# Performance work log

Measured on AMD Instinct MI355X. Metric: run time of the kernel, lower is better.

Reference implementation:

```python
import jax, jax.numpy as jnp
import numpy as np

H, W = 64, 64
C = 256
NH = 8
WS = 8
SS = 4
N = WS * WS
HD = C // NH
HIDDEN = 4 * C
CPB_HIDDEN = 512
EPS = 1e-6


def _window_partition(x, ws):
    B, H_, W_, C_ = x.shape
    x = x.reshape(B, H_ // ws, ws, W_ // ws, ws, C_).transpose(0, 1, 3, 2, 4, 5)
    return x.reshape(-1, ws, ws, C_)


def _window_reverse(win, ws, H_, W_):
    B = win.shape[0] // ((H_ // ws) * (W_ // ws))
    x = win.reshape(B, H_ // ws, W_ // ws, ws, ws, -1).transpose(0, 1, 3, 2, 4, 5)
    return x.reshape(B, H_, W_, -1)


def _coords_table():
    # (1, 2*WS-1, 2*WS-1, 2) log-spaced continuous relative coords (SwinV2 CPB)
    ch = np.arange(-(WS - 1), WS)
    cw = np.arange(-(WS - 1), WS)
    t = np.stack(np.meshgrid(ch, cw, indexing='ij'), axis=-1)[None].astype(np.float32)
    t = t / (WS - 1) * 8.0
    t = np.sign(t) * np.log2(np.abs(t) + 1.0) / np.log2(8.0)
    return t.astype(np.float32)


def _rpe_index():
    coords = np.stack(np.meshgrid(np.arange(WS), np.arange(WS), indexing='ij'))
    cf = coords.reshape(2, -1)
    rel = (cf[:, :, None] - cf[:, None, :]).transpose(1, 2, 0)
    rel[:, :, 0] += WS - 1
    rel[:, :, 1] += WS - 1
    rel[:, :, 0] *= 2 * WS - 1
    return rel.sum(-1)  # (N, N) int


def _attn_mask():
    img = np.zeros((1, H, W, 1), np.float32)
    cnt = 0
    for hs in (slice(0, -WS), slice(-WS, -SS), slice(-SS, None)):
        for ws_ in (slice(0, -WS), slice(-WS, -SS), slice(-SS, None)):
            img[:, hs, ws_, :] = cnt
            cnt += 1
    mw = img.reshape(1, H // WS, WS, W // WS, WS, 1).transpose(0, 1, 3, 2, 4, 5).reshape(-1, N)
    am = mw[:, None, :] - mw[:, :, None]
    return np.where(am != 0, -100.0, 0.0).astype(np.float32)  # (nW, N, N)


_TABLE = jnp.asarray(_coords_table())
_RPE = jnp.asarray(_rpe_index().reshape(-1))
_AMASK = jnp.asarray(_attn_mask())


def setup_inputs() -> dict:
    key = jax.random.key(0)
    ks = jax.random.split(key, 12)
    s = 0.02
    return {
        'x': jax.random.normal(ks[0], (32, H * W, C), jnp.float32),
        'qkv_w': jax.random.normal(ks[1], (C, 3 * C), jnp.float32) * s,
        'q_bias': jnp.zeros((C,), jnp.float32),
        'v_bias': jnp.zeros((C,), jnp.float32),
        'logit_scale': jnp.log(10.0 * jnp.ones((NH, 1, 1), jnp.float32)),
        'cpb_w1': jax.random.normal(ks[2], (2, CPB_HIDDEN), jnp.float32) * s,
        'cpb_b1': jnp.zeros((CPB_HIDDEN,), jnp.float32),
        'cpb_w2': jax.random.normal(ks[3], (CPB_HIDDEN, NH), jnp.float32) * s,
        'proj_w': jax.random.normal(ks[4], (C, C), jnp.float32) * s,
        'proj_b': jnp.zeros((C,), jnp.float32),
        'norm1_scale': jnp.ones((C,), jnp.float32),
        'norm1_bias': jnp.zeros((C,), jnp.float32),
        'norm2_scale': jnp.ones((C,), jnp.float32),
        'norm2_bias': jnp.zeros((C,), jnp.float32),
        'fc1_w': jax.random.normal(ks[5], (C, HIDDEN), jnp.float32) * s,
        'fc1_b': jnp.zeros((HIDDEN,), jnp.float32),
        'fc2_w': jax.random.normal(ks[6], (HIDDEN, C), jnp.float32) * s,
        'fc2_b': jnp.zeros((C,), jnp.float32),
    }


def _layernorm(y, scale, bias):
    mu = jnp.mean(y, axis=-1, keepdims=True)
    var = jnp.mean(jnp.square(y - mu), axis=-1, keepdims=True)
    return (y - mu) * jax.lax.rsqrt(var + EPS) * scale + bias


def _l2n(t):
    return t * jax.lax.rsqrt(jnp.maximum(jnp.sum(t * t, axis=-1, keepdims=True), 1e-12))


def reference(x, qkv_w, q_bias, v_bias, logit_scale, cpb_w1, cpb_b1, cpb_w2,
              proj_w, proj_b, norm1_scale, norm1_bias, norm2_scale, norm2_bias,
              fc1_w, fc1_b, fc2_w, fc2_b):
    B, L, C_ = x.shape
    nW = _AMASK.shape[0]
    shortcut = x

    # cyclic shift + window partition
    xi = x.reshape(B, H, W, C_)
    xi = jnp.roll(xi, (-SS, -SS), axis=(1, 2))
    xw = _window_partition(xi, WS).reshape(-1, N, C_)  # (B_, N, C)
    B_ = xw.shape[0]

    # qkv with q/v bias only (k bias is zero)
    qkv_bias = jnp.concatenate([q_bias, jnp.zeros_like(v_bias), v_bias])
    qkv = xw @ qkv_w + qkv_bias
    qkv = qkv.reshape(B_, N, 3, NH, HD).transpose(2, 0, 3, 1, 4)
    q, k, v = qkv[0], qkv[1], qkv[2]  # (B_, NH, N, HD)

    # cosine attention with learned clamped logit scale
    attn = jnp.einsum('bhnd,bhmd->bhnm', _l2n(q), _l2n(k))
    scale = jnp.exp(jnp.minimum(logit_scale, np.log(100.0)))  # (NH,1,1)
    attn = attn * scale

    # continuous-position-bias MLP -> relative position bias, 16*sigmoid
    bias_table = jax.nn.relu(_TABLE @ cpb_w1 + cpb_b1) @ cpb_w2  # (1,2WS-1,2WS-1,NH)
    bias_table = bias_table.reshape(-1, NH)
    rpb = bias_table[_RPE].reshape(N, N, NH).transpose(2, 0, 1)  # (NH,N,N)
    attn = attn + (16.0 * jax.nn.sigmoid(rpb))[None]

    # shifted-window mask
    attn = attn.reshape(B_ // nW, nW, NH, N, N) + _AMASK[None, :, None]
    attn = jax.nn.softmax(attn.reshape(B_, NH, N, N), axis=-1)

    out = jnp.einsum('bhnm,bhmd->bnhd', attn, v).reshape(B_, N, C_)
    out = out @ proj_w + proj_b

    # window reverse + reverse cyclic shift
    out = _window_reverse(out.reshape(-1, WS, WS, C_), WS, H, W)
    out = jnp.roll(out, (SS, SS), axis=(1, 2)).reshape(B, L, C_)

    # SwinV2 post-norm residuals
    x1 = shortcut + _layernorm(out, norm1_scale, norm1_bias)
    h = jax.nn.gelu(x1 @ fc1_w + fc1_b) @ fc2_w + fc2_b
    return x1 + _layernorm(h, norm2_scale, norm2_bias)
```

## Files before the change

kernel.cpp:

```cpp
#include <hip/hip_runtime.h>

typedef __bf16 bf16;
typedef __bf16 bf16x8 __attribute__((ext_vector_type(8)));
typedef __bf16 bf16x4 __attribute__((ext_vector_type(4)));
typedef float  f32x4  __attribute__((ext_vector_type(4)));

#define MFMA16(a, b, c) __builtin_amdgcn_mfma_f32_16x16x32_bf16(a, b, c, 0, 0, 0)

__device__ __forceinline__ void gload_lds16(const void* g, void* l) {
    __builtin_amdgcn_global_load_lds((const __attribute__((address_space(1))) void*)g,
                                     (__attribute__((address_space(3))) void*)l, 16, 0, 0);
}

__device__ __forceinline__ long win2orig(long r) {
    long b = r >> 12; int rem = (int)(r & 4095);
    int widx = rem >> 6, t = rem & 63;
    int rp = ((widx >> 3) << 3) + (t >> 3), cp = ((widx & 7) << 3) + (t & 7);
    int rr = (rp + 4) & 63, cc = (cp + 4) & 63;
    return (b << 12) + rr * 64 + cc;
}

template <int GELU>
__global__ __launch_bounds__(256) void gemm_bt(const bf16* __restrict__ A,
                                               const bf16* __restrict__ Bt,
                                               const float* __restrict__ bias,
                                               bf16* __restrict__ C,
                                               int M, int N, int K) {
    __shared__ bf16 As[4096];
    __shared__ bf16 Bs[4096];
    const int t = threadIdx.x;
    const int w = t >> 6, l = t & 63;
    const int l15 = l & 15, q4 = l >> 4;
    const int wm = w >> 1, wn = w & 1;
    const long row0 = (long)blockIdx.y * 128;
    const int col0 = blockIdx.x * 128;

    const bf16* aP = A + (row0 + w * 16 + l15) * (long)K + q4 * 8;
    const bf16* bP = Bt + (long)(col0 + w * 16 + l15) * K + q4 * 8;
    const long step64 = 64L * K;

    f32x4 acc[4][4];
#pragma unroll
    for (int i = 0; i < 4; i++)
#pragma unroll
        for (int j = 0; j < 4; j++)
#pragma unroll
            for (int r = 0; r < 4; r++) acc[i][j][r] = 0.f;

    const int KT = K >> 5;
    for (int kt = 0; kt < KT; ++kt) {
        __syncthreads();
        gload_lds16(aP,          &As[w * 512]);
        gload_lds16(aP + step64, &As[w * 512 + 2048]);
        gload_lds16(bP,          &Bs[w * 512]);
        gload_lds16(bP + step64, &Bs[w * 512 + 2048]);
        aP += 32; bP += 32;
        __syncthreads();
        bf16x8 af[4], bfv[4];
#pragma unroll
        for (int mi = 0; mi < 4; mi++) af[mi] = *(const bf16x8*)(&As[(wm * 4 + mi) * 512 + l * 8]);
#pragma unroll
        for (int nj = 0; nj < 4; nj++) bfv[nj] = *(const bf16x8*)(&Bs[(wn * 4 + nj) * 512 + l * 8]);
#pragma unroll
        for (int mi = 0; mi < 4; mi++)
#pragma unroll
            for (int nj = 0; nj < 4; nj++) acc[mi][nj] = MFMA16(af[mi], bfv[nj], acc[mi][nj]);
    }

    float cb[4];
#pragma unroll
    for (int nj = 0; nj < 4; nj++) cb[nj] = bias[col0 + wn * 64 + nj * 16 + l15];

#pragma unroll
    for (int mi = 0; mi < 4; mi++) {
#pragma unroll
        for (int reg = 0; reg < 4; reg++) {
            long r = row0 + wm * 64 + mi * 16 + q4 * 4 + reg;
            bf16* cpn = C + r * (long)N + col0 + wn * 64 + l15;
#pragma unroll
            for (int nj = 0; nj < 4; nj++) {
                float v = acc[mi][nj][reg] + cb[nj];
                if (GELU) {
                    float u = 0.7978845608028654f * (v + 0.044715f * v * v * v);
                    float e = __expf(2.f * u);
                    float th = 1.f - 2.f / (e + 1.f);
                    v = 0.5f * v * (1.f + th);
                }
                cpn[nj * 16] = (bf16)v;
            }
        }
    }
}

__global__ __launch_bounds__(64) void attn_kernel(const bf16* __restrict__ qkv,
                                                  const float* __restrict__ bias16,
                                                  const float* __restrict__ logit_scale,
                                                  bf16* __restrict__ outp) {
    __shared__ bf16 P[64 * 72];
    __shared__ bf16 Vt[32 * 72];
    const int unit = blockIdx.x;
    const int w = unit >> 3, h = unit & 7;
    const int l = threadIdx.x;
    const int l15 = l & 15, q4 = l >> 4;
    const bf16* base = qkv + (long)w * 64 * 768;

    {
        const bf16* vp = base + l * 768 + 512 + h * 32;
#pragma unroll
        for (int c = 0; c < 4; c++) {
            bf16x8 vv = *(const bf16x8*)(vp + c * 8);
#pragma unroll
            for (int j = 0; j < 8; j++) Vt[(c * 8 + j) * 72 + l] = vv[j];
        }
    }

    const float scale = __expf(fminf(logit_scale[h], 4.605170186f));

    bf16x8 qf[4], kf[4];
#pragma unroll
    for (int mi = 0; mi < 4; mi++) {
        const bf16* p = base + (mi * 16 + l15) * 768 + h * 32 + q4 * 8;
        bf16x8 xv = *(const bf16x8*)p;
        float fv[8]; float ss = 0.f;
#pragma unroll
        for (int j = 0; j < 8; j++) { fv[j] = (float)xv[j]; ss += fv[j] * fv[j]; }
        ss += __shfl_xor(ss, 16); ss += __shfl_xor(ss, 32);
        float rs = rsqrtf(fmaxf(ss, 1e-12f));
#pragma unroll
        for (int j = 0; j < 8; j++) qf[mi][j] = (bf16)(fv[j] * rs);
    }
#pragma unroll
    for (int nj = 0; nj < 4; nj++) {
        const bf16* p = base + (nj * 16 + l15) * 768 + 256 + h * 32 + q4 * 8;
        bf16x8 xv = *(const bf16x8*)p;
        float fv[8]; float ss = 0.f;
#pragma unroll
        for (int j = 0; j < 8; j++) { fv[j] = (float)xv[j]; ss += fv[j] * fv[j]; }
        ss += __shfl_xor(ss, 16); ss += __shfl_xor(ss, 32);
        float rs = rsqrtf(fmaxf(ss, 1e-12f));
#pragma unroll
        for (int j = 0; j < 8; j++) kf[nj][j] = (bf16)(fv[j] * rs);
    }

    f32x4 acc[4][4];
#pragma unroll
    for (int i = 0; i < 4; i++)
#pragma unroll
        for (int j = 0; j < 4; j++)
#pragma unroll
            for (int r = 0; r < 4; r++) acc[i][j][r] = 0.f;
#pragma unroll
    for (int mi = 0; mi < 4; mi++)
#pragma unroll
        for (int nj = 0; nj < 4; nj++) acc[mi][nj] = MFMA16(qf[mi], kf[nj], acc[mi][nj]);

    const int widx = w & 63, wr = widx >> 3, wc = widx & 7;
    const bool edge = (wr == 7) || (wc == 7);
    int crid[4];
    if (edge) {
#pragma unroll
        for (int nj = 0; nj < 4; nj++) {
            int m = nj * 16 + l15;
            int R = wr * 8 + (m >> 3), Cc = wc * 8 + (m & 7);
            crid[nj] = ((R < 56) ? 0 : (R < 60 ? 1 : 2)) * 3 + ((Cc < 56) ? 0 : (Cc < 60 ? 1 : 2));
        }
    }
    const float* bh = bias16 + h * 4096;
#pragma unroll
    for (int mi = 0; mi < 4; mi++) {
#pragma unroll
        for (int reg = 0; reg < 4; reg++) {
            int n = mi * 16 + q4 * 4 + reg;
            const float* bp = bh + n * 64;
            int nrid = 0;
            if (edge) {
                int R = wr * 8 + (n >> 3), Cc = wc * 8 + (n & 7);
                nrid = ((R < 56) ? 0 : (R < 60 ? 1 : 2)) * 3 + ((Cc < 56) ? 0 : (Cc < 60 ? 1 : 2));
            }
#pragma unroll
            for (int nj = 0; nj < 4; nj++) {
                float v = acc[mi][nj][reg] * scale + bp[nj * 16 + l15];
                if (edge && nrid != crid[nj]) v -= 100.f;
                acc[mi][nj][reg] = v;
            }
        }
    }

#pragma unroll
    for (int mi = 0; mi < 4; mi++) {
#pragma unroll
        for (int reg = 0; reg < 4; reg++) {
            float mx = fmaxf(fmaxf(acc[mi][0][reg], acc[mi][1][reg]),
                             fmaxf(acc[mi][2][reg], acc[mi][3][reg]));
            mx = fmaxf(mx, __shfl_xor(mx, 1));
            mx = fmaxf(mx, __shfl_xor(mx, 2));
            mx = fmaxf(mx, __shfl_xor(mx, 4));
            mx = fmaxf(mx, __shfl_xor(mx, 8));
            float s = 0.f;
#pragma unroll
            for (int nj = 0; nj < 4; nj++) {
                float e = __expf(acc[mi][nj][reg] - mx);
                acc[mi][nj][reg] = e; s += e;
            }
            s += __shfl_xor(s, 1); s += __shfl_xor(s, 2);
            s += __shfl_xor(s, 4); s += __shfl_xor(s, 8);
            float inv = 1.f / s;
            int n = mi * 16 + q4 * 4 + reg;
#pragma unroll
            for (int nj = 0; nj < 4; nj++)
                P[n * 72 + nj * 16 + l15] = (bf16)(acc[mi][nj][reg] * inv);
        }
    }
    __syncthreads();

    f32x4 o[4][2];
#pragma unroll
    for (int i = 0; i < 4; i++)
#pragma unroll
        for (int j = 0; j < 2; j++)
#pragma unroll
            for (int r = 0; r < 4; r++) o[i][j][r] = 0.f;
#pragma unroll
    for (int ks = 0; ks < 2; ks++) {
        bf16x8 vf[2];
#pragma unroll
        for (int nj = 0; nj < 2; nj++) vf[nj] = *(const bf16x8*)(&Vt[(nj * 16 + l15) * 72 + ks * 32 + q4 * 8]);
#pragma unroll
        for (int mi = 0; mi < 4; mi++) {
            bf16x8 pf = *(const bf16x8*)(&P[(mi * 16 + l15) * 72 + ks * 32 + q4 * 8]);
#pragma unroll
            for (int nj = 0; nj < 2; nj++) o[mi][nj] = MFMA16(pf, vf[nj], o[mi][nj]);
        }
    }

    bf16* op = outp + (long)w * 64 * 256 + h * 32;
#pragma unroll
    for (int mi = 0; mi < 4; mi++)
#pragma unroll
        for (int reg = 0; reg < 4; reg++) {
            int tok = mi * 16 + q4 * 4 + reg;
#pragma unroll
            for (int nj = 0; nj < 2; nj++)
                op[tok * 256 + nj * 16 + l15] = (bf16)o[mi][nj][reg];
        }
}

__global__ __launch_bounds__(256) void norm1_kernel(const bf16* __restrict__ pin,
                                                    const float* __restrict__ x,
                                                    const float* __restrict__ g,
                                                    const float* __restrict__ bb,
                                                    bf16* __restrict__ x1h) {
    const int tid = threadIdx.x;
    const int wid = tid >> 6, l = tid & 63;
    const long rl = (long)blockIdx.x * 4 + wid;
    bf16x4 v4 = *(const bf16x4*)(pin + rl * 256 + l * 4);
    float v[4]; float s = 0.f, sq = 0.f;
#pragma unroll
    for (int c = 0; c < 4; c++) { v[c] = (float)v4[c]; s += v[c]; sq += v[c] * v[c]; }
#pragma unroll
    for (int off = 1; off < 64; off <<= 1) { s += __shfl_xor(s, off); sq += __shfl_xor(sq, off); }
    float mu = s * 0.00390625f;
    float var = sq * 0.00390625f - mu * mu;
    float rstd = rsqrtf(var + 1e-6f);
    long orig = win2orig(rl);
    float4 xv = *(const float4*)(x + orig * 256 + l * 4);
    float4 gv = *(const float4*)(g + l * 4);
    float4 bv = *(const float4*)(bb + l * 4);
    bf16x4 oh;
    oh[0] = (bf16)(xv.x + ((v[0] - mu) * rstd * gv.x + bv.x));
    oh[1] = (bf16)(xv.y + ((v[1] - mu) * rstd * gv.y + bv.y));
    oh[2] = (bf16)(xv.z + ((v[2] - mu) * rstd * gv.z + bv.z));
    oh[3] = (bf16)(xv.w + ((v[3] - mu) * rstd * gv.w + bv.w));
    *(bf16x4*)(x1h + orig * 256 + l * 4) = oh;
}

__global__ __launch_bounds__(256) void norm2_kernel(const bf16* __restrict__ hin,
                                                    const bf16* __restrict__ x1h,
                                                    const float* __restrict__ g,
                                                    const float* __restrict__ bb,
                                                    float* __restrict__ outp) {
    const int tid = threadIdx.x;
    const int wid = tid >> 6, l = tid & 63;
    const long rl = (long)blockIdx.x * 4 + wid;
    bf16x4 v4 = *(const bf16x4*)(hin + rl * 256 + l * 4);
    float v[4]; float s = 0.f, sq = 0.f;
#pragma unroll
    for (int c = 0; c < 4; c++) { v[c] = (float)v4[c]; s += v[c]; sq += v[c] * v[c]; }
#pragma unroll
    for (int off = 1; off < 64; off <<= 1) { s += __shfl_xor(s, off); sq += __shfl_xor(sq, off); }
    float mu = s * 0.00390625f;
    float var = sq * 0.00390625f - mu * mu;
    float rstd = rsqrtf(var + 1e-6f);
    bf16x4 xv4 = *(const bf16x4*)(x1h + rl * 256 + l * 4);
    float4 gv = *(const float4*)(g + l * 4);
    float4 bv = *(const float4*)(bb + l * 4);
    float4 ov;
    ov.x = (float)xv4[0] + ((v[0] - mu) * rstd * gv.x + bv.x);
    ov.y = (float)xv4[1] + ((v[1] - mu) * rstd * gv.y + bv.y);
    ov.z = (float)xv4[2] + ((v[2] - mu) * rstd * gv.z + bv.z);
    ov.w = (float)xv4[3] + ((v[3] - mu) * rstd * gv.w + bv.w);
    *(float4*)(outp + rl * 256 + l * 4) = ov;
}

__global__ __launch_bounds__(256) void gather_cast(const float* __restrict__ x,
                                                   bf16* __restrict__ out) {
    const int tid = threadIdx.x;
    const int wid = tid >> 6, l = tid & 63;
    const long rl = (long)blockIdx.x * 4 + wid;
    long orig = win2orig(rl);
    float4 v = *(const float4*)(x + orig * 256 + l * 4);
    bf16x4 o = {(bf16)v.x, (bf16)v.y, (bf16)v.z, (bf16)v.w};
    *(bf16x4*)(out + rl * 256 + l * 4) = o;
}

__global__ void transpose_cast(const float* __restrict__ in, bf16* __restrict__ out, int K, int N) {
    int id = blockIdx.x * 256 + threadIdx.x;
    if (id < K * N) {
        int n = id / K, k = id - n * K;
        out[id] = (bf16)in[k * N + n];
    }
}

__global__ void build_qkv_bias(const float* __restrict__ qb, const float* __restrict__ vb,
                               float* __restrict__ out) {
    int i = blockIdx.x * 256 + threadIdx.x;
    if (i < 768) out[i] = (i < 256) ? qb[i] : ((i < 512) ? 0.f : vb[i - 512]);
}

__device__ __forceinline__ float cpcoord(int d) {
    float v = (float)d * (8.0f / 7.0f);
    float r = log2f(fabsf(v) + 1.0f) * (1.0f / 3.0f);
    return v < 0.f ? -r : r;
}

__global__ void cpb1(const float* __restrict__ w1, const float* __restrict__ b1,
                     const float* __restrict__ w2, float* __restrict__ tbl) {
    int a = threadIdx.x;
    if (a >= 225) return;
    int i = a / 15, j = a - i * 15;
    float t0 = cpcoord(i - 7), t1 = cpcoord(j - 7);
    float acc[8];
#pragma unroll
    for (int o = 0; o < 8; o++) acc[o] = 0.f;
    for (int jj = 0; jj < 512; jj++) {
        float hv = fmaf(t0, w1[jj], fmaf(t1, w1[512 + jj], b1[jj]));
        hv = fmaxf(hv, 0.f);
#pragma unroll
        for (int o = 0; o < 8; o++) acc[o] = fmaf(hv, w2[jj * 8 + o], acc[o]);
    }
#pragma unroll
    for (int o = 0; o < 8; o++) tbl[a * 8 + o] = acc[o];
}

__global__ void cpb2(const float* __restrict__ tbl, float* __restrict__ bias16) {
    int id = blockIdx.x * 256 + threadIdx.x;
    if (id >= 32768) return;
    int h = id >> 12, n = (id >> 6) & 63, m = id & 63;
    int r0 = (n >> 3) - (m >> 3) + 7;
    int r1 = (n & 7) - (m & 7) + 7;
    float v = tbl[(r0 * 15 + r1) * 8 + h];
    bias16[id] = 16.f / (1.f + __expf(-v));
}

extern "C" void kernel_launch(void* const* d_in, const int* in_sizes, int n_in,
                              void* d_out, int out_size, void* d_ws, size_t ws_size,
                              hipStream_t stream) {
    const float* x   = (const float*)d_in[0];
    const float* qkvw= (const float*)d_in[1];
    const float* qb  = (const float*)d_in[2];
    const float* vb  = (const float*)d_in[3];
    const float* ls  = (const float*)d_in[4];
    const float* cw1 = (const float*)d_in[5];
    const float* cb1 = (const float*)d_in[6];
    const float* cw2 = (const float*)d_in[7];
    const float* pw  = (const float*)d_in[8];
    const float* pb  = (const float*)d_in[9];
    const float* n1s = (const float*)d_in[10];
    const float* n1b = (const float*)d_in[11];
    const float* n2s = (const float*)d_in[12];
    const float* n2b = (const float*)d_in[13];
    const float* f1w = (const float*)d_in[14];
    const float* f1b = (const float*)d_in[15];
    const float* f2w = (const float*)d_in[16];
    const float* f2b = (const float*)d_in[17];

    char* ws = (char*)d_ws;
    if (ws_size < 471859200UL) return;
    bf16*  qkvBt   = (bf16*)(ws + 0);
    bf16*  projBt  = (bf16*)(ws + 393216);
    bf16*  fc1Bt   = (bf16*)(ws + 524288);
    bf16*  fc2Bt   = (bf16*)(ws + 1048576);
    float* qkvBias = (float*)(ws + 1572864);
    float* cpbTbl  = (float*)(ws + 1575936);
    float* bias16  = (float*)(ws + 1583360);
    bf16* xbf     = (bf16*)(ws + 2097152);
    bf16* qkvBuf  = (bf16*)(ws + 69206016);
    bf16* attnOut = (bf16*)(ws + 270532608);
    bf16* projOut = (bf16*)(ws + 337641472);
    bf16* x1h     = (bf16*)(ws + 404750336);
    bf16* hBuf    = (bf16*)(ws + 2097152);
    bf16* fc2Out  = (bf16*)(ws + 337641472);

    transpose_cast<<<768, 256, 0, stream>>>(qkvw, qkvBt, 256, 768);
    transpose_cast<<<256, 256, 0, stream>>>(pw, projBt, 256, 256);
    transpose_cast<<<1024, 256, 0, stream>>>(f1w, fc1Bt, 256, 1024);
    transpose_cast<<<1024, 256, 0, stream>>>(f2w, fc2Bt, 1024, 256);
    build_qkv_bias<<<3, 256, 0, stream>>>(qb, vb, qkvBias);
    cpb1<<<1, 256, 0, stream>>>(cw1, cb1, cw2, cpbTbl);
    cpb2<<<128, 256, 0, stream>>>(cpbTbl, bias16);

    gather_cast<<<32768, 256, 0, stream>>>(x, xbf);
    gemm_bt<0><<<dim3(6, 1024), 256, 0, stream>>>(xbf, qkvBt, qkvBias, qkvBuf, 131072, 768, 256);
    attn_kernel<<<16384, 64, 0, stream>>>(qkvBuf, bias16, ls, attnOut);
    gemm_bt<0><<<dim3(2, 1024), 256, 0, stream>>>(attnOut, projBt, pb, projOut, 131072, 256, 256);
    norm1_kernel<<<32768, 256, 0, stream>>>(projOut, x, n1s, n1b, x1h);
    gemm_bt<1><<<dim3(8, 1024), 256, 0, stream>>>(x1h, fc1Bt, f1b, hBuf, 131072, 1024, 256);
    gemm_bt<0><<<dim3(2, 1024), 256, 0, stream>>>(hBuf, fc2Bt, f2b, fc2Out, 131072, 256, 1024);
    norm2_kernel<<<32768, 256, 0, stream>>>(fc2Out, x1h, n2s, n2b, (float*)d_out);
}
```

Baseline: 1.057 ms.

## Double-buffer GEMM LDS tiles, swizzle workgroup order, and simplify GELU

The GEMM kernel now uses two LDS buffers. It prefetches the next K-slice with global_load_lds while MFMAs run on the current one, which cuts the loop to one barrier per iteration. Workgroup IDs are remapped with an 8-way swizzle to improve L2 reuse of the operand tiles. The tanh-form GELU is rewritten algebraically as v*sigmoid(2u) using the hardware exp2 and reciprocal instructions. The costs are double the LDS use, which may lower occupancy, and slightly lower GELU precision from the approximate rcp.

```diff
diff --git a/kernel.cpp b/kernel.cpp
--- a/kernel.cpp
+++ b/kernel.cpp
@@ -26,14 +26,21 @@
                                                const float* __restrict__ bias,
                                                bf16* __restrict__ C,
                                                int M, int N, int K) {
-    __shared__ bf16 As[4096];
-    __shared__ bf16 Bs[4096];
+    __shared__ bf16 As[2][4096];
+    __shared__ bf16 Bs[2][4096];
     const int t = threadIdx.x;
     const int w = t >> 6, l = t & 63;
     const int l15 = l & 15, q4 = l >> 4;
     const int wm = w >> 1, wn = w & 1;
-    const long row0 = (long)blockIdx.y * 128;
-    const int col0 = blockIdx.x * 128;
+
+    const unsigned gx = gridDim.x;
+    const unsigned nwg = gx * gridDim.y;
+    const unsigned id0 = blockIdx.y * gx + blockIdx.x;
+    const unsigned swz = (id0 & 7u) * (nwg >> 3) + (id0 >> 3);
+    const unsigned bx = swz % gx, by = swz / gx;
+
+    const long row0 = (long)by * 128;
+    const int col0 = (int)bx * 128;
 
     const bf16* aP = A + (row0 + w * 16 + l15) * (long)K + q4 * 8;
     const bf16* bP = Bt + (long)(col0 + w * 16 + l15) * K + q4 * 8;
@@ -48,23 +55,34 @@
             for (int r = 0; r < 4; r++) acc[i][j][r] = 0.f;
 
     const int KT = K >> 5;
+
+    gload_lds16(aP,          &As[0][w * 512]);
+    gload_lds16(aP + step64, &As[0][w * 512 + 2048]);
+    gload_lds16(bP,          &Bs[0][w * 512]);
+    gload_lds16(bP + step64, &Bs[0][w * 512 + 2048]);
+    aP += 32; bP += 32;
+    __syncthreads();
+
+    int cur = 0;
     for (int kt = 0; kt < KT; ++kt) {
+        if (kt + 1 < KT) {
+            gload_lds16(aP,          &As[cur ^ 1][w * 512]);
+            gload_lds16(aP + step64, &As[cur ^ 1][w * 512 + 2048]);
+            gload_lds16(bP,          &Bs[cur ^ 1][w * 512]);
+            gload_lds16(bP + step64, &Bs[cur ^ 1][w * 512 + 2048]);
+            aP += 32; bP += 32;
+        }
+        bf16x8 af[4], bfv[4];
+#pragma unroll
+        for (int mi = 0; mi < 4; mi++) af[mi] = *(const bf16x8*)(&As[cur][(wm * 4 + mi) * 512 + l * 8]);
+#pragma unroll
+        for (int nj = 0; nj < 4; nj++) bfv[nj] = *(const bf16x8*)(&Bs[cur][(wn * 4 + nj) * 512 + l * 8]);
+#pragma unroll
+        for (int mi = 0; mi < 4; mi++)
+#pragma unroll
+            for (int nj = 0; nj < 4; nj++) acc[mi][nj] = MFMA16(af[mi], bfv[nj], acc[mi][nj]);
         __syncthreads();
-        gload_lds16(aP,          &As[w * 512]);
-        gload_lds16(aP + step64, &As[w * 512 + 2048]);
-        gload_lds16(bP,          &Bs[w * 512]);
-        gload_lds16(bP + step64, &Bs[w * 512 + 2048]);
-        aP += 32; bP += 32;
-        __syncthreads();
-        bf16x8 af[4], bfv[4];
-#pragma unroll
-        for (int mi = 0; mi < 4; mi++) af[mi] = *(const bf16x8*)(&As[(wm * 4 + mi) * 512 + l * 8]);
-#pragma unroll
-        for (int nj = 0; nj < 4; nj++) bfv[nj] = *(const bf16x8*)(&Bs[(wn * 4 + nj) * 512 + l * 8]);
-#pragma unroll
-        for (int mi = 0; mi < 4; mi++)
-#pragma unroll
-            for (int nj = 0; nj < 4; nj++) acc[mi][nj] = MFMA16(af[mi], bfv[nj], acc[mi][nj]);
+        cur ^= 1;
     }
 
     float cb[4];
@@ -81,10 +99,10 @@
             for (int nj = 0; nj < 4; nj++) {
                 float v = acc[mi][nj][reg] + cb[nj];
                 if (GELU) {
-                    float u = 0.7978845608028654f * (v + 0.044715f * v * v * v);
-                    float e = __expf(2.f * u);
-                    float th = 1.f - 2.f / (e + 1.f);
-                    v = 0.5f * v * (1.f + th);
+                    float v2 = v * v;
+                    float tt = v * fmaf(v2, -0.10294702f, -2.30218094f);
+                    float e = __builtin_amdgcn_exp2f(tt);
+                    v = v * __builtin_amdgcn_rcpf(1.f + e);
                 }
                 cpn[nj * 16] = (bf16)v;
             }
```

New measurement: 1.039 ms. About the same (-1.8%).
